# Kernel optimization log

Measured on AMD Instinct MI355X. Metric: run time of the kernel, lower is better.

The kernel has to match this reference:

```python
import jax, jax.numpy as jnp
import numpy as np

NT, NH, NW = 16, 16, 16
HEADS, DIM_HEAD = 8, 64
DIM = 512
DEPTH = 4
EPS = 1e-5


def _layernorm(x, g, b):
    mu = jnp.mean(x, axis=-1, keepdims=True)
    var = jnp.mean(jnp.square(x - mu), axis=-1, keepdims=True)
    return (x - mu) * jax.lax.rsqrt(var + EPS) * g + b


def setup_inputs() -> dict:
    key = jax.random.key(0)
    ks = jax.random.split(key, 4)
    n = NT * NH * NW
    inner = HEADS * DIM_HEAD
    x = jax.random.normal(ks[0], (8, n, DIM), dtype=jnp.float32)
    Wqkv = jax.random.normal(ks[1], (DEPTH, DIM, 3 * inner), dtype=jnp.float32) * (DIM ** -0.5)
    Wout = jax.random.normal(ks[2], (DEPTH, inner, DIM), dtype=jnp.float32) * (inner ** -0.5)
    bout = jnp.zeros((DEPTH, DIM), dtype=jnp.float32)
    gamma = jnp.ones((DEPTH, DIM), dtype=jnp.float32)
    beta = jnp.zeros((DEPTH, DIM), dtype=jnp.float32)
    return {"x": x, "Wqkv": Wqkv, "Wout": Wout, "bout": bout, "gamma": gamma, "beta": beta}


def _fda_layer(x, Wqkv, Wout, bout, g, bb):
    b, n, d = x.shape
    hs = HEADS // 2
    s = NH * NW
    scale = DIM_HEAD ** -0.5
    y = _layernorm(x, g, bb)
    qkv = y @ Wqkv  # (b, n, 3*inner)
    q, k, v = jnp.split(qkv, 3, axis=-1)
    # b n (h d) -> b h n d
    def to_heads(t):
        return t.reshape(b, n, HEADS, DIM_HEAD).transpose(0, 2, 1, 3)
    q, k, v = to_heads(q), to_heads(k), to_heads(v)
    # spatial branch: first half of heads, view n as (t, s)
    qs = q[:, :hs].reshape(b, hs, NT, s, DIM_HEAD)
    ks = k[:, :hs].reshape(b, hs, NT, s, DIM_HEAD)
    vs = v[:, :hs].reshape(b, hs, NT, s, DIM_HEAD)
    sp_dots = jnp.einsum('bhtid,bhtjd->bhtij', qs, ks) * scale
    sp_attn = jax.nn.softmax(sp_dots, axis=-1)
    sp_out = jnp.einsum('bhtij,bhtjd->bhtid', sp_attn, vs)  # (b,hs,nt,s,dh)
    # temporal branch: second half of heads, view n as (s, t)
    qt = q[:, hs:].reshape(b, hs, s, NT, DIM_HEAD)
    kt = k[:, hs:].reshape(b, hs, s, NT, DIM_HEAD)
    vt = v[:, hs:].reshape(b, hs, s, NT, DIM_HEAD)
    tp_dots = jnp.einsum('bhsid,bhsjd->bhsij', qt, kt) * scale
    tp_attn = jax.nn.softmax(tp_dots, axis=-1)
    tp_out = jnp.einsum('bhsij,bhsjd->bhsid', tp_attn, vt)  # (b,hs,s,nt,dh)
    out = jnp.concatenate([sp_out.reshape(b, hs, n, DIM_HEAD),
                           tp_out.reshape(b, hs, n, DIM_HEAD)], axis=1)  # (b,h,n,dh)
    out = out.transpose(0, 2, 1, 3).reshape(b, n, HEADS * DIM_HEAD)
    return out @ Wout + bout


def reference(x, Wqkv, Wout, bout, gamma, beta):
    for l in range(DEPTH):
        x = _fda_layer(x, Wqkv[l], Wout[l], bout[l], gamma[l], beta[l]) + x
    return x
```

## Files before the change

kernel.cpp:

```cpp
#include <hip/hip_runtime.h>
#include <hip/hip_bf16.h>

typedef __bf16 bf16x8 __attribute__((ext_vector_type(8)));
typedef float f32x4 __attribute__((ext_vector_type(4)));

#define AS1(p) ((const __attribute__((address_space(1))) void*)(p))
#define AS3(p) ((__attribute__((address_space(3))) void*)(p))

__global__ __launch_bounds__(256) void transpose32(const float* __restrict__ W,
                                                   __bf16* __restrict__ WT,
                                                   int K, int N) {
  __shared__ float t[32][33];
  int l = blockIdx.z;
  int k0 = blockIdx.y * 32, n0 = blockIdx.x * 32;
  int tx = threadIdx.x & 31, ty = threadIdx.x >> 5;
  const float* src = W + ((size_t)l * K + k0) * N + n0;
#pragma unroll
  for (int i = 0; i < 32; i += 8) t[ty + i][tx] = src[(size_t)(ty + i) * N + tx];
  __syncthreads();
  __bf16* dst = WT + ((size_t)l * N + n0) * K + k0;
#pragma unroll
  for (int i = 0; i < 32; i += 8) dst[(size_t)(ty + i) * K + tx] = (__bf16)t[tx][ty + i];
}

__global__ __launch_bounds__(256) void ln_kernel(const float* __restrict__ x,
                                                 const float* __restrict__ gamma,
                                                 const float* __restrict__ beta,
                                                 __bf16* __restrict__ y) {
  int wave = threadIdx.x >> 6, lane = threadIdx.x & 63;
  size_t row = (size_t)blockIdx.x * 4 + wave;
  const float* xr = x + row * 512 + lane * 8;
  float4 v0 = *(const float4*)xr;
  float4 v1 = *(const float4*)(xr + 4);
  float s = v0.x + v0.y + v0.z + v0.w + v1.x + v1.y + v1.z + v1.w;
  float ss = v0.x * v0.x + v0.y * v0.y + v0.z * v0.z + v0.w * v0.w +
             v1.x * v1.x + v1.y * v1.y + v1.z * v1.z + v1.w * v1.w;
#pragma unroll
  for (int m = 1; m < 64; m <<= 1) {
    s += __shfl_xor(s, m);
    ss += __shfl_xor(ss, m);
  }
  float mean = s * (1.f / 512.f);
  float var = ss * (1.f / 512.f) - mean * mean;
  float rstd = rsqrtf(var + 1e-5f);
  const float* gp = gamma + lane * 8;
  const float* bp = beta + lane * 8;
  float4 g0 = *(const float4*)gp, g1 = *(const float4*)(gp + 4);
  float4 b0 = *(const float4*)bp, b1 = *(const float4*)(bp + 4);
  bf16x8 o;
  o[0] = (__bf16)((v0.x - mean) * rstd * g0.x + b0.x);
  o[1] = (__bf16)((v0.y - mean) * rstd * g0.y + b0.y);
  o[2] = (__bf16)((v0.z - mean) * rstd * g0.z + b0.z);
  o[3] = (__bf16)((v0.w - mean) * rstd * g0.w + b0.w);
  o[4] = (__bf16)((v1.x - mean) * rstd * g1.x + b1.x);
  o[5] = (__bf16)((v1.y - mean) * rstd * g1.y + b1.y);
  o[6] = (__bf16)((v1.z - mean) * rstd * g1.z + b1.z);
  o[7] = (__bf16)((v1.w - mean) * rstd * g1.w + b1.w);
  *(bf16x8*)(y + row * 512 + lane * 8) = o;
}

#define STAGE_PART(kt_, part_)                                                   \
  {                                                                              \
    const __bf16* gb_ = ((part_) < 2) ? Abase : Bbase;                           \
    int rowoff_ = ((part_)&1) * 128;                                             \
    const __bf16* g0_ = gb_ + (size_t)(rowoff_ + r0s) * 512 + (kt_)*64 + s0 * 8; \
    const __bf16* g1_ = gb_ + (size_t)(rowoff_ + r1s) * 512 + (kt_)*64 + s1 * 8; \
    char* lb_ = lds + (((kt_)&1) * 65536) + ((part_)*16384);                     \
    __builtin_amdgcn_global_load_lds(AS1(g0_), AS3(lb_ + ldsw0), 16, 0, 0);      \
    __builtin_amdgcn_global_load_lds(AS1(g1_), AS3(lb_ + ldsw1), 16, 0, 0);      \
  }

template <int NCOLS>
__global__ __launch_bounds__(512, 2) void gemm256(const __bf16* __restrict__ A,
                                                  const __bf16* __restrict__ BT,
                                                  __bf16* __restrict__ Cb) {
  extern __shared__ __attribute__((aligned(128))) char lds[];
  constexpr int NT = NCOLS / 256;
  int bid = blockIdx.x;
  int cpx = gridDim.x >> 3;
  int L = (bid & 7) * cpx + (bid >> 3);
  int tileM = L / NT, tileN = L - tileM * NT;
  int tid = threadIdx.x;
  int l = tid & 63, w = tid >> 6;
  int lm = l & 15, lh = l >> 4;
  int wave_m = w >> 2, wave_n = w & 3;
  const __bf16* Abase = A + (size_t)tileM * 256 * 512;
  const __bf16* Bbase = BT + (size_t)tileN * 256 * 512;
  int r0s = tid >> 3, s0 = (tid & 7) ^ (r0s & 7);
  int p1 = tid + 512;
  int r1s = p1 >> 3, s1 = (p1 & 7) ^ (r1s & 7);
  int ldsw0 = (w * 64) * 16, ldsw1 = (512 + w * 64) * 16;

  f32x4 acc[8][4];
#pragma unroll
  for (int m = 0; m < 8; ++m)
#pragma unroll
    for (int n = 0; n < 4; ++n) acc[m][n] = (f32x4){0.f, 0.f, 0.f, 0.f};

  int xorv = (lm & 7) << 4;
  int kb0 = (lh * 16) ^ xorv;
  int kb1 = (64 + lh * 16) ^ xorv;
  int arow = wave_m * 128 + lm;
  int brow = wave_n * 64 + lm;

  STAGE_PART(0, 0); STAGE_PART(0, 1); STAGE_PART(0, 2); STAGE_PART(0, 3);

  for (int kt = 0; kt < 8; ++kt) {
    char* sb = lds + (kt & 1) * 65536;
    if (kt < 7) {
      STAGE_PART(kt + 1, 0);
      asm volatile("s_waitcnt vmcnt(2)" ::: "memory");
    } else {
      asm volatile("s_waitcnt vmcnt(0)" ::: "memory");
    }
    __builtin_amdgcn_sched_barrier(0);
    __builtin_amdgcn_s_barrier();
    bf16x8 bfrag[4][2];
#pragma unroll
    for (int nf = 0; nf < 4; ++nf) {
      const char* bp = sb + 32768 + (brow + nf * 16) * 128;
      bfrag[nf][0] = *(const bf16x8*)(bp + kb0);
      bfrag[nf][1] = *(const bf16x8*)(bp + kb1);
    }
#pragma unroll
    for (int ph = 0; ph < 4; ++ph) {
      bf16x8 af[2][2];
#pragma unroll
      for (int m = 0; m < 2; ++m) {
        const char* ap = sb + (arow + (ph * 2 + m) * 16) * 128;
        af[m][0] = *(const bf16x8*)(ap + kb0);
        af[m][1] = *(const bf16x8*)(ap + kb1);
      }
      if (ph == 1 && kt < 7) STAGE_PART(kt + 1, 1);
      if (ph == 2 && kt < 7) STAGE_PART(kt + 1, 2);
      if (ph == 3 && kt < 7) STAGE_PART(kt + 1, 3);
      __builtin_amdgcn_s_barrier();
      __builtin_amdgcn_s_setprio(1);
#pragma unroll
      for (int m = 0; m < 2; ++m)
#pragma unroll
        for (int nf = 0; nf < 4; ++nf) {
          acc[ph * 2 + m][nf] = __builtin_amdgcn_mfma_f32_16x16x32_bf16(
              af[m][0], bfrag[nf][0], acc[ph * 2 + m][nf], 0, 0, 0);
          acc[ph * 2 + m][nf] = __builtin_amdgcn_mfma_f32_16x16x32_bf16(
              af[m][1], bfrag[nf][1], acc[ph * 2 + m][nf], 0, 0, 0);
        }
      __builtin_amdgcn_s_setprio(0);
    }
    __builtin_amdgcn_s_barrier();
  }

  int crow = tileM * 256 + wave_m * 128 + lh * 4;
  int ccol = tileN * 256 + wave_n * 64 + lm;
#pragma unroll
  for (int mf = 0; mf < 8; ++mf)
#pragma unroll
    for (int nf = 0; nf < 4; ++nf) {
      int col = ccol + nf * 16;
#pragma unroll
      for (int r = 0; r < 4; ++r) {
        size_t idx = (size_t)(crow + mf * 16 + r) * NCOLS + col;
        Cb[idx] = (__bf16)acc[mf][nf][r];
      }
    }
}

#define STAGE_PART128(kt_, part_)                                               \
  {                                                                             \
    const __bf16* gb_ = ((part_) < 2) ? Abase : Bbase;                          \
    int rowoff_ = ((part_)&1) * 64;                                             \
    const __bf16* g0_ = gb_ + (size_t)(rowoff_ + r0s) * 512 + (kt_)*64 + s0 * 8;\
    const __bf16* g1_ = gb_ + (size_t)(rowoff_ + r1s) * 512 + (kt_)*64 + s1 * 8;\
    char* lb_ = lds + (((kt_)&1) * 32768) + (((part_) < 2) ? 0 : 16384) +       \
                ((part_)&1) * 8192;                                             \
    __builtin_amdgcn_global_load_lds(AS1(g0_), AS3(lb_ + ldsw0), 16, 0, 0);     \
    __builtin_amdgcn_global_load_lds(AS1(g1_), AS3(lb_ + ldsw1), 16, 0, 0);     \
  }

__global__ __launch_bounds__(256, 2) void gemm128res(const __bf16* __restrict__ A,
                                                     const __bf16* __restrict__ BT,
                                                     float* Cf,
                                                     const float* __restrict__ bias,
                                                     const float* Resid) {
  extern __shared__ __attribute__((aligned(128))) char lds[];
  constexpr int NCOLS = 512;
  constexpr int NT = 4;
  int bid = blockIdx.x;
  int cpx = gridDim.x >> 3;
  int L = (bid & 7) * cpx + (bid >> 3);
  int tileM = L / NT, tileN = L - tileM * NT;
  int tid = threadIdx.x;
  int l = tid & 63, w = tid >> 6;
  int lm = l & 15, lh = l >> 4;
  int wave_m = w >> 1, wave_n = w & 1;
  const __bf16* Abase = A + (size_t)tileM * 128 * 512;
  const __bf16* Bbase = BT + (size_t)tileN * 128 * 512;
  int r0s = tid >> 3, s0 = (tid & 7) ^ (r0s & 7);
  int p1 = tid + 256;
  int r1s = p1 >> 3, s1 = (p1 & 7) ^ (r1s & 7);
  int ldsw0 = (w * 64) * 16, ldsw1 = (256 + w * 64) * 16;

  f32x4 acc[4][4];
#pragma unroll
  for (int m = 0; m < 4; ++m)
#pragma unroll
    for (int n = 0; n < 4; ++n) acc[m][n] = (f32x4){0.f, 0.f, 0.f, 0.f};

  int xorv = (lm & 7) << 4;
  int kb0 = (lh * 16) ^ xorv;
  int kb1 = (64 + lh * 16) ^ xorv;
  int arow = wave_m * 64 + lm;
  int brow = wave_n * 64 + lm;

  STAGE_PART128(0, 0); STAGE_PART128(0, 1); STAGE_PART128(0, 2); STAGE_PART128(0, 3);

  for (int kt = 0; kt < 8; ++kt) {
    char* sb = lds + (kt & 1) * 32768;
    if (kt < 7) {
      STAGE_PART128(kt + 1, 0);
      asm volatile("s_waitcnt vmcnt(2)" ::: "memory");
    } else {
      asm volatile("s_waitcnt vmcnt(0)" ::: "memory");
    }
    __builtin_amdgcn_sched_barrier(0);
    __builtin_amdgcn_s_barrier();
    bf16x8 bfrag[4][2];
#pragma unroll
    for (int nf = 0; nf < 4; ++nf) {
      const char* bp = sb + 16384 + (brow + nf * 16) * 128;
      bfrag[nf][0] = *(const bf16x8*)(bp + kb0);
      bfrag[nf][1] = *(const bf16x8*)(bp + kb1);
    }
#pragma unroll
    for (int ph = 0; ph < 4; ++ph) {
      bf16x8 af0, af1;
      {
        const char* ap = sb + (arow + ph * 16) * 128;
        af0 = *(const bf16x8*)(ap + kb0);
        af1 = *(const bf16x8*)(ap + kb1);
      }
      if (ph == 1 && kt < 7) STAGE_PART128(kt + 1, 1);
      if (ph == 2 && kt < 7) STAGE_PART128(kt + 1, 2);
      if (ph == 3 && kt < 7) STAGE_PART128(kt + 1, 3);
      __builtin_amdgcn_s_barrier();
      __builtin_amdgcn_s_setprio(1);
#pragma unroll
      for (int nf = 0; nf < 4; ++nf) {
        acc[ph][nf] = __builtin_amdgcn_mfma_f32_16x16x32_bf16(af0, bfrag[nf][0],
                                                              acc[ph][nf], 0, 0, 0);
        acc[ph][nf] = __builtin_amdgcn_mfma_f32_16x16x32_bf16(af1, bfrag[nf][1],
                                                              acc[ph][nf], 0, 0, 0);
      }
      __builtin_amdgcn_s_setprio(0);
    }
    __builtin_amdgcn_s_barrier();
  }

  float* lf = (float*)(lds + w * 8192);
  int crow0 = tileM * 128 + wave_m * 64;
  int ccol0 = tileN * 128 + wave_n * 64;
  int erow = l >> 2;
  int ecl = (l & 3) * 4;
  float4 b4[4];
#pragma unroll
  for (int j = 0; j < 4; ++j)
    b4[j] = *(const float4*)(bias + ccol0 + ecl + j * 16);
#pragma unroll
  for (int mf = 0; mf < 4; ++mf) {
#pragma unroll
    for (int nf = 0; nf < 4; ++nf)
#pragma unroll
      for (int r = 0; r < 4; ++r)
        lf[(lh * 4 + r) * 68 + nf * 16 + lm] = acc[mf][nf][r];
    size_t rowg = (size_t)(crow0 + mf * 16 + erow);
    const float* rp = Resid + rowg * NCOLS + ccol0 + ecl;
    float* cp = Cf + rowg * NCOLS + ccol0 + ecl;
#pragma unroll
    for (int j = 0; j < 4; ++j) {
      float4 a4 = *(float4*)&lf[erow * 68 + ecl + j * 16];
      float4 r4 = *(const float4*)(rp + j * 16);
      float4 o4;
      o4.x = a4.x + b4[j].x + r4.x;
      o4.y = a4.y + b4[j].y + r4.y;
      o4.z = a4.z + b4[j].z + r4.z;
      o4.w = a4.w + b4[j].w + r4.w;
      *(float4*)(cp + j * 16) = o4;
    }
  }
}

__global__ __launch_bounds__(256) void attn_spatial(const __bf16* __restrict__ qkv,
                                                    __bf16* __restrict__ attn_out) {
  __shared__ __attribute__((aligned(16))) __bf16 VT[64 * 256];
  __shared__ __attribute__((aligned(16))) __bf16 P[4][4096];
  int bid = blockIdx.x;
  int b = bid >> 6;
  int rem = bid & 63;
  int h = rem >> 4;
  int t = rem & 15;
  int tid = threadIdx.x;
  int w = tid >> 6, l = tid & 63;
  size_t nbase = (size_t)b * 4096 + t * 256;
#pragma unroll
  for (int i = 0; i < 8; i++) {
    int idx = tid + i * 256;
    int key = idx >> 3, dseg = idx & 7;
    bf16x8 v = *(const bf16x8*)(qkv + (nbase + key) * 1536 + 1024 + h * 64 + dseg * 8);
#pragma unroll
    for (int d2 = 0; d2 < 8; d2++) {
      int dh = dseg * 8 + d2;
      VT[dh * 256 + (((key >> 3) ^ (dh & 7)) << 3) + (key & 7)] = v[d2];
    }
  }
  __syncthreads();
  int lm = l & 15, lh = l >> 4;
  for (int it = 0; it < 4; ++it) {
    int qbase = it * 64 + w * 16;
    const __bf16* qp = qkv + (nbase + qbase + lm) * 1536 + h * 64 + lh * 8;
    bf16x8 aq0 = *(const bf16x8*)qp;
    bf16x8 aq1 = *(const bf16x8*)(qp + 32);
    f32x4 sa[16];
#pragma unroll
    for (int tn = 0; tn < 16; ++tn) {
      const __bf16* kp = qkv + (nbase + tn * 16 + lm) * 1536 + 512 + h * 64 + lh * 8;
      bf16x8 bk0 = *(const bf16x8*)kp;
      bf16x8 bk1 = *(const bf16x8*)(kp + 32);
      f32x4 z = {0.f, 0.f, 0.f, 0.f};
      z = __builtin_amdgcn_mfma_f32_16x16x32_bf16(aq0, bk0, z, 0, 0, 0);
      sa[tn] = __builtin_amdgcn_mfma_f32_16x16x32_bf16(aq1, bk1, z, 0, 0, 0);
    }
    float rmax[4] = {-1e30f, -1e30f, -1e30f, -1e30f};
#pragma unroll
    for (int tn = 0; tn < 16; ++tn)
#pragma unroll
      for (int r = 0; r < 4; ++r) {
        sa[tn][r] *= 0.125f;
        rmax[r] = fmaxf(rmax[r], sa[tn][r]);
      }
#pragma unroll
    for (int m = 1; m < 16; m <<= 1)
#pragma unroll
      for (int r = 0; r < 4; ++r) rmax[r] = fmaxf(rmax[r], __shfl_xor(rmax[r], m));
    float rsum[4] = {0.f, 0.f, 0.f, 0.f};
#pragma unroll
    for (int tn = 0; tn < 16; ++tn)
#pragma unroll
      for (int r = 0; r < 4; ++r) {
        float e = __expf(sa[tn][r] - rmax[r]);
        sa[tn][r] = e;
        rsum[r] += e;
      }
#pragma unroll
    for (int m = 1; m < 16; m <<= 1)
#pragma unroll
      for (int r = 0; r < 4; ++r) rsum[r] += __shfl_xor(rsum[r], m);
    float rinv[4];
#pragma unroll
    for (int r = 0; r < 4; ++r) rinv[r] = 1.f / rsum[r];
#pragma unroll
    for (int tn = 0; tn < 16; ++tn)
#pragma unroll
      for (int r = 0; r < 4; ++r) {
        int row = lh * 4 + r;
        int col = tn * 16 + lm;
        P[w][row * 256 + ((((col >> 3)) ^ (row & 7)) << 3) + (col & 7)] =
            (__bf16)(sa[tn][r] * rinv[r]);
      }
    f32x4 oa[4];
#pragma unroll
    for (int nt = 0; nt < 4; ++nt) oa[nt] = (f32x4){0.f, 0.f, 0.f, 0.f};
#pragma unroll
    for (int kc = 0; kc < 8; ++kc) {
      bf16x8 pa = *(const bf16x8*)&P[w][lm * 256 + (((kc * 4 + lh) ^ (lm & 7)) << 3)];
#pragma unroll
      for (int nt = 0; nt < 4; ++nt) {
        int dh = nt * 16 + lm;
        bf16x8 bv = *(const bf16x8*)&VT[dh * 256 + (((kc * 4 + lh) ^ (dh & 7)) << 3)];
        oa[nt] = __builtin_amdgcn_mfma_f32_16x16x32_bf16(pa, bv, oa[nt], 0, 0, 0);
      }
    }
#pragma unroll
    for (int nt = 0; nt < 4; ++nt)
#pragma unroll
      for (int r = 0; r < 4; ++r) {
        size_t row = nbase + qbase + lh * 4 + r;
        attn_out[row * 512 + h * 64 + nt * 16 + lm] = (__bf16)oa[nt][r];
      }
  }
}

__global__ __launch_bounds__(256) void attn_temporal(const __bf16* __restrict__ qkv,
                                                     __bf16* __restrict__ attn_out) {
  __shared__ __attribute__((aligned(16))) __bf16 VT[4][64 * 40];
  __shared__ __attribute__((aligned(16))) __bf16 P[4][16 * 40];
  int tid = threadIdx.x;
  {
    float4 z4 = {0.f, 0.f, 0.f, 0.f};
#pragma unroll
    for (int i = 0; i < 5; ++i) ((float4*)&VT[0][0])[tid + i * 256] = z4;
    if (tid < 64) ((float4*)&P[0][0])[tid + 256] = z4;
    ((float4*)&P[0][0])[tid] = z4;
  }
  __syncthreads();
  int bid = blockIdx.x;
  int b = bid >> 8;
  int rem = bid & 255;
  int h = 4 + (rem >> 6);
  int g = rem & 63;
  int w = tid >> 6, l = tid & 63;
  int lm = l & 15, lh = l >> 4;
  int sid = g * 4 + w;
  size_t n0 = (size_t)b * 4096 + sid * 16;

  const __bf16* qp = qkv + (n0 + lm) * 1536 + h * 64 + lh * 8;
  bf16x8 aq0 = *(const bf16x8*)qp;
  bf16x8 aq1 = *(const bf16x8*)(qp + 32);
  const __bf16* kp = qp + 512;
  bf16x8 bk0 = *(const bf16x8*)kp;
  bf16x8 bk1 = *(const bf16x8*)(kp + 32);
  int kk = l >> 2;
  int dh0 = (l & 3) * 8;
  const __bf16* vp = qkv + (n0 + kk) * 1536 + 1024 + h * 64 + dh0;
  bf16x8 vr0 = *(const bf16x8*)vp;
  bf16x8 vr1 = *(const bf16x8*)(vp + 32);

  f32x4 s4 = {0.f, 0.f, 0.f, 0.f};
  s4 = __builtin_amdgcn_mfma_f32_16x16x32_bf16(aq0, bk0, s4, 0, 0, 0);
  s4 = __builtin_amdgcn_mfma_f32_16x16x32_bf16(aq1, bk1, s4, 0, 0, 0);

#pragma unroll
  for (int d2 = 0; d2 < 8; ++d2) VT[w][(dh0 + d2) * 40 + kk] = vr0[d2];
#pragma unroll
  for (int d2 = 0; d2 < 8; ++d2) VT[w][(dh0 + 32 + d2) * 40 + kk] = vr1[d2];

  float e[4];
  float rmax[4];
#pragma unroll
  for (int r = 0; r < 4; ++r) {
    e[r] = s4[r] * 0.125f;
    rmax[r] = e[r];
  }
#pragma unroll
  for (int m = 1; m < 16; m <<= 1)
#pragma unroll
    for (int r = 0; r < 4; ++r) rmax[r] = fmaxf(rmax[r], __shfl_xor(rmax[r], m));
  float rsum[4];
#pragma unroll
  for (int r = 0; r < 4; ++r) {
    e[r] = __expf(e[r] - rmax[r]);
    rsum[r] = e[r];
  }
#pragma unroll
  for (int m = 1; m < 16; m <<= 1)
#pragma unroll
    for (int r = 0; r < 4; ++r) rsum[r] += __shfl_xor(rsum[r], m);
#pragma unroll
  for (int r = 0; r < 4; ++r)
    P[w][(lh * 4 + r) * 40 + lm] = (__bf16)(e[r] / rsum[r]);

  asm volatile("s_waitcnt lgkmcnt(0)" ::: "memory");
  __builtin_amdgcn_sched_barrier(0);

  bf16x8 pa = *(const bf16x8*)&P[w][lm * 40 + lh * 8];
#pragma unroll
  for (int nt = 0; nt < 4; ++nt) {
    bf16x8 bv = *(const bf16x8*)&VT[w][(nt * 16 + lm) * 40 + lh * 8];
    f32x4 oa = {0.f, 0.f, 0.f, 0.f};
    oa = __builtin_amdgcn_mfma_f32_16x16x32_bf16(pa, bv, oa, 0, 0, 0);
#pragma unroll
    for (int r = 0; r < 4; ++r)
      attn_out[(n0 + lh * 4 + r) * 512 + h * 64 + nt * 16 + lm] = (__bf16)oa[r];
  }
}

extern "C" void kernel_launch(void* const* d_in, const int* in_sizes, int n_in,
                              void* d_out, int out_size, void* d_ws, size_t ws_size,
                              hipStream_t stream) {
  const float* x = (const float*)d_in[0];
  const float* Wqkv = (const float*)d_in[1];
  const float* Wout = (const float*)d_in[2];
  const float* bout = (const float*)d_in[3];
  const float* gamma = (const float*)d_in[4];
  const float* beta = (const float*)d_in[5];
  float* out = (float*)d_out;

  const size_t OFF_WOUT = 6291456;
  const size_t OFF_Y = OFF_WOUT + 2097152;
  const size_t OFF_QKV = OFF_Y + 33554432;
  const size_t NEEDED = OFF_QKV + 100663296;
  if (ws_size < NEEDED) return;
  char* ws = (char*)d_ws;
  __bf16* WqkvT = (__bf16*)ws;
  __bf16* WoutT = (__bf16*)(ws + OFF_WOUT);
  __bf16* ybuf = (__bf16*)(ws + OFF_Y);
  __bf16* qkv = (__bf16*)(ws + OFF_QKV);

  hipFuncSetAttribute((const void*)gemm256<1536>,
                      hipFuncAttributeMaxDynamicSharedMemorySize, 131072);
  hipFuncSetAttribute((const void*)gemm128res,
                      hipFuncAttributeMaxDynamicSharedMemorySize, 65536);

  transpose32<<<dim3(48, 16, 4), 256, 0, stream>>>(Wqkv, WqkvT, 512, 1536);
  transpose32<<<dim3(16, 16, 4), 256, 0, stream>>>(Wout, WoutT, 512, 512);

  for (int layer = 0; layer < 4; ++layer) {
    const float* src = (layer == 0) ? x : out;
    ln_kernel<<<8192, 256, 0, stream>>>(src, gamma + layer * 512, beta + layer * 512, ybuf);
    gemm256<1536><<<768, 512, 131072, stream>>>(
        ybuf, WqkvT + (size_t)layer * 1536 * 512, qkv);
    attn_spatial<<<512, 256, 0, stream>>>(qkv, ybuf);
    attn_temporal<<<2048, 256, 0, stream>>>(qkv, ybuf);
    gemm128res<<<1024, 256, 65536, stream>>>(
        ybuf, WoutT + (size_t)layer * 512 * 512, out, bout + layer * 512, src);
  }
}
```

Before: 667.5 us.

## Use 8 waves per block in output-projection GEMM with smaller per-wave tiles

The residual output-projection GEMM now runs 512 threads (8 waves in a 2x4 grid) per 128x128 tile instead of 4 waves, so each wave computes a 64x32 sub-tile. Staging is simplified to two parts per k-step (A and B halves), and the fine-grained per-phase barriers are replaced by loading all A fragments up front and then issuing the MFMAs in one burst. The intent is more latency hiding through higher wave occupancy and fewer barriers. The cost is more LDS fragment reads per MFMA and more register pressure from the launch bound.

```diff
diff --git a/kernel.cpp b/kernel.cpp
--- a/kernel.cpp
+++ b/kernel.cpp
@@ -165,19 +165,17 @@
     }
 }
 
-#define STAGE_PART128(kt_, part_)                                               \
+#define STAGE128(kt_, part_)                                                    \
   {                                                                             \
-    const __bf16* gb_ = ((part_) < 2) ? Abase : Bbase;                          \
-    int rowoff_ = ((part_)&1) * 64;                                             \
-    const __bf16* g0_ = gb_ + (size_t)(rowoff_ + r0s) * 512 + (kt_)*64 + s0 * 8;\
-    const __bf16* g1_ = gb_ + (size_t)(rowoff_ + r1s) * 512 + (kt_)*64 + s1 * 8;\
-    char* lb_ = lds + (((kt_)&1) * 32768) + (((part_) < 2) ? 0 : 16384) +       \
-                ((part_)&1) * 8192;                                             \
+    const __bf16* gb_ = ((part_) == 0) ? Abase : Bbase;                         \
+    const __bf16* g0_ = gb_ + (size_t)r0s * 512 + (kt_)*64 + s0 * 8;            \
+    const __bf16* g1_ = gb_ + (size_t)r1s * 512 + (kt_)*64 + s1 * 8;            \
+    char* lb_ = lds + (((kt_)&1) * 32768) + ((part_)*16384);                    \
     __builtin_amdgcn_global_load_lds(AS1(g0_), AS3(lb_ + ldsw0), 16, 0, 0);     \
     __builtin_amdgcn_global_load_lds(AS1(g1_), AS3(lb_ + ldsw1), 16, 0, 0);     \
   }
 
-__global__ __launch_bounds__(256, 2) void gemm128res(const __bf16* __restrict__ A,
+__global__ __launch_bounds__(512, 4) void gemm128res(const __bf16* __restrict__ A,
                                                      const __bf16* __restrict__ BT,
                                                      float* Cf,
                                                      const float* __restrict__ bias,
@@ -192,100 +190,95 @@
   int tid = threadIdx.x;
   int l = tid & 63, w = tid >> 6;
   int lm = l & 15, lh = l >> 4;
-  int wave_m = w >> 1, wave_n = w & 1;
+  int wave_m = w >> 2, wave_n = w & 3;
   const __bf16* Abase = A + (size_t)tileM * 128 * 512;
   const __bf16* Bbase = BT + (size_t)tileN * 128 * 512;
   int r0s = tid >> 3, s0 = (tid & 7) ^ (r0s & 7);
-  int p1 = tid + 256;
+  int p1 = tid + 512;
   int r1s = p1 >> 3, s1 = (p1 & 7) ^ (r1s & 7);
-  int ldsw0 = (w * 64) * 16, ldsw1 = (256 + w * 64) * 16;
-
-  f32x4 acc[4][4];
+  int ldsw0 = (w * 64) * 16, ldsw1 = 8192 + (w * 64) * 16;
+
+  f32x4 acc[4][2];
 #pragma unroll
   for (int m = 0; m < 4; ++m)
 #pragma unroll
-    for (int n = 0; n < 4; ++n) acc[m][n] = (f32x4){0.f, 0.f, 0.f, 0.f};
+    for (int n = 0; n < 2; ++n) acc[m][n] = (f32x4){0.f, 0.f, 0.f, 0.f};
 
   int xorv = (lm & 7) << 4;
   int kb0 = (lh * 16) ^ xorv;
   int kb1 = (64 + lh * 16) ^ xorv;
   int arow = wave_m * 64 + lm;
-  int brow = wave_n * 64 + lm;
-
-  STAGE_PART128(0, 0); STAGE_PART128(0, 1); STAGE_PART128(0, 2); STAGE_PART128(0, 3);
+  int brow = wave_n * 32 + lm;
+
+  STAGE128(0, 0); STAGE128(0, 1);
 
   for (int kt = 0; kt < 8; ++kt) {
     char* sb = lds + (kt & 1) * 32768;
     if (kt < 7) {
-      STAGE_PART128(kt + 1, 0);
+      STAGE128(kt + 1, 0);
       asm volatile("s_waitcnt vmcnt(2)" ::: "memory");
     } else {
       asm volatile("s_waitcnt vmcnt(0)" ::: "memory");
     }
     __builtin_amdgcn_sched_barrier(0);
     __builtin_amdgcn_s_barrier();
-    bf16x8 bfrag[4][2];
-#pragma unroll
-    for (int nf = 0; nf < 4; ++nf) {
+    bf16x8 bfrag[2][2];
+#pragma unroll
+    for (int nf = 0; nf < 2; ++nf) {
       const char* bp = sb + 16384 + (brow + nf * 16) * 128;
       bfrag[nf][0] = *(const bf16x8*)(bp + kb0);
       bfrag[nf][1] = *(const bf16x8*)(bp + kb1);
     }
-#pragma unroll
-    for (int ph = 0; ph < 4; ++ph) {
-      bf16x8 af0, af1;
-      {
-        const char* ap = sb + (arow + ph * 16) * 128;
-        af0 = *(const bf16x8*)(ap + kb0);
-        af1 = *(const bf16x8*)(ap + kb1);
-      }
-      if (ph == 1 && kt < 7) STAGE_PART128(kt + 1, 1);
-      if (ph == 2 && kt < 7) STAGE_PART128(kt + 1, 2);
-      if (ph == 3 && kt < 7) STAGE_PART128(kt + 1, 3);
-      __builtin_amdgcn_s_barrier();
-      __builtin_amdgcn_s_setprio(1);
-#pragma unroll
-      for (int nf = 0; nf < 4; ++nf) {
-        acc[ph][nf] = __builtin_amdgcn_mfma_f32_16x16x32_bf16(af0, bfrag[nf][0],
-                                                              acc[ph][nf], 0, 0, 0);
-        acc[ph][nf] = __builtin_amdgcn_mfma_f32_16x16x32_bf16(af1, bfrag[nf][1],
-                                                              acc[ph][nf], 0, 0, 0);
-      }
-      __builtin_amdgcn_s_setprio(0);
-    }
+    bf16x8 af[4][2];
+#pragma unroll
+    for (int mf = 0; mf < 4; ++mf) {
+      const char* ap = sb + (arow + mf * 16) * 128;
+      af[mf][0] = *(const bf16x8*)(ap + kb0);
+      af[mf][1] = *(const bf16x8*)(ap + kb1);
+    }
+    if (kt < 7) STAGE128(kt + 1, 1);
+    __builtin_amdgcn_s_setprio(1);
+#pragma unroll
+    for (int mf = 0; mf < 4; ++mf)
+#pragma unroll
+      for (int nf = 0; nf < 2; ++nf) {
+        acc[mf][nf] = __builtin_amdgcn_mfma_f32_16x16x32_bf16(af[mf][0], bfrag[nf][0],
+                                                              acc[mf][nf], 0, 0, 0);
+        acc[mf][nf] = __builtin_amdgcn_mfma_f32_16x16x32_bf16(af[mf][1], bfrag[nf][1],
+                                                              acc[mf][nf], 0, 0, 0);
+      }
+    __builtin_amdgcn_s_setprio(0);
     __builtin_amdgcn_s_barrier();
   }
 
-  float* lf = (float*)(lds + w * 8192);
+  float* lf = (float*)(lds + w * 2560);
   int crow0 = tileM * 128 + wave_m * 64;
-  int ccol0 = tileN * 128 + wave_n * 64;
+  int ccol0 = tileN * 128 + wave_n * 32;
   int erow = l >> 2;
-  int ecl = (l & 3) * 4;
-  float4 b4[4];
-#pragma unroll
-  for (int j = 0; j < 4; ++j)
-    b4[j] = *(const float4*)(bias + ccol0 + ecl + j * 16);
+  int ecl = (l & 3) * 8;
+  float4 ba = *(const float4*)(bias + ccol0 + ecl);
+  float4 bb = *(const float4*)(bias + ccol0 + ecl + 4);
 #pragma unroll
   for (int mf = 0; mf < 4; ++mf) {
 #pragma unroll
-    for (int nf = 0; nf < 4; ++nf)
+    for (int nf = 0; nf < 2; ++nf)
 #pragma unroll
       for (int r = 0; r < 4; ++r)
-        lf[(lh * 4 + r) * 68 + nf * 16 + lm] = acc[mf][nf][r];
+        lf[(lh * 4 + r) * 40 + nf * 16 + lm] = acc[mf][nf][r];
     size_t rowg = (size_t)(crow0 + mf * 16 + erow);
     const float* rp = Resid + rowg * NCOLS + ccol0 + ecl;
     float* cp = Cf + rowg * NCOLS + ccol0 + ecl;
-#pragma unroll
-    for (int j = 0; j < 4; ++j) {
-      float4 a4 = *(float4*)&lf[erow * 68 + ecl + j * 16];
-      float4 r4 = *(const float4*)(rp + j * 16);
-      float4 o4;
-      o4.x = a4.x + b4[j].x + r4.x;
-      o4.y = a4.y + b4[j].y + r4.y;
-      o4.z = a4.z + b4[j].z + r4.z;
-      o4.w = a4.w + b4[j].w + r4.w;
-      *(float4*)(cp + j * 16) = o4;
-    }
+    float4 a0 = *(float4*)&lf[erow * 40 + ecl];
+    float4 a1 = *(float4*)&lf[erow * 40 + ecl + 4];
+    float4 r0 = *(const float4*)rp;
+    float4 r1 = *(const float4*)(rp + 4);
+    float4 o0, o1;
+    o0.x = a0.x + ba.x + r0.x; o0.y = a0.y + ba.y + r0.y;
+    o0.z = a0.z + ba.z + r0.z; o0.w = a0.w + ba.w + r0.w;
+    o1.x = a1.x + bb.x + r1.x; o1.y = a1.y + bb.y + r1.y;
+    o1.z = a1.z + bb.z + r1.z; o1.w = a1.w + bb.w + r1.w;
+    *(float4*)cp = o0;
+    *(float4*)(cp + 4) = o1;
   }
 }
 
@@ -510,7 +503,7 @@
         ybuf, WqkvT + (size_t)layer * 1536 * 512, qkv);
     attn_spatial<<<512, 256, 0, stream>>>(qkv, ybuf);
     attn_temporal<<<2048, 256, 0, stream>>>(qkv, ybuf);
-    gemm128res<<<1024, 256, 65536, stream>>>(
+    gemm128res<<<1024, 512, 65536, stream>>>(
         ybuf, WoutT + (size_t)layer * 512 * 512, out, bout + layer * 512, src);
   }
 }
```

Measured after the change: 659.1 us. About the same (-1.3%).
